# Optimization experiments

Measured on AMD Instinct MI355X. Metric: run time of the kernel, lower is better.

## Reference

```python
import jax, jax.numpy as jnp
import numpy as np

ANNEALING_SCALE = 0.1
BS, NV, S, D, V = 2, 16, 1024, 768, 50257

def setup_inputs() -> dict:
    key = jax.random.key(0)
    k1, k2, k3, k4, k5 = jax.random.split(key, 5)
    return {
        "input_ids": jax.random.randint(k1, (BS, S), 0, V),
        "content": jax.random.normal(k2, (BS, NV, S, D), dtype=jnp.float32),
        "contextualization": jax.random.normal(k3, (BS, NV, S, S), dtype=jnp.float32) * 0.05,
        "lm_head_weight": jax.random.normal(k4, (V, D), dtype=jnp.float32) * 0.02,
        "content_weights": jax.random.uniform(k5, (V, NV), dtype=jnp.float32),
    }

def reference(input_ids, content, contextualization, lm_head_weight, content_weights):
    bs, nv, s, d = content.shape
    # --- mask_annealing ---
    # Original computes relu(content @ W.T) over full vocab then gathers at input_ids.
    # Equivalent: gather rows of W first, then contract (same math since relu is
    # elementwise and only gathered columns are summed).
    Wg = lm_head_weight[input_ids]                              # (bs, s, d)
    sims = jnp.einsum('bkid,bjd->bkij', content, Wg)            # (bs, 16, s, s)
    sims = jnp.sum(jax.nn.relu(sims), axis=3)                   # (bs, 16, s)
    scores = jax.nn.sigmoid(-ANNEALING_SCALE * sims + 6.0)
    # upweight_nearby modifier
    scores = scores * (1.0 + jnp.arange(s, dtype=content.dtype) / 100.0)[None, None, :]
    scores = jnp.transpose(scores, (0, 2, 1))                   # (bs, s, 16)
    # --- create_content_soft_mask ---
    cw = content_weights[input_ids]                             # (bs, s, 16)
    weights = cw * scores + (1.0 - scores)                      # (bs, s, 16)
    # --- weighted sense combination ---
    content_m = content * jnp.transpose(weights, (0, 2, 1))[..., None]  # (bs,16,s,d)
    hidden = jnp.einsum('bkij,bkjd->bid', contextualization, content_m) # (bs, s, d)
    logits = hidden @ lm_head_weight.T                          # (bs, s, vocab)
    return logits
```

## Files before the change

### kernel.cpp

```cpp
#include <hip/hip_runtime.h>
#include <cstdint>
#include <cstddef>

#define BSZ 2
#define NV 16
#define SEQ 1024
#define DIM 768
#define VOC 50257
#define VOCP 50304

typedef unsigned int u32;
typedef unsigned short u16;
typedef _Float16 half8 __attribute__((ext_vector_type(8)));
typedef float f32x4 __attribute__((ext_vector_type(4)));

__device__ __forceinline__ u16 f2h(float f) {
  return __builtin_bit_cast(unsigned short, (_Float16)f);
}
__device__ __forceinline__ u32 pk2h(float a, float b) {
  return (u32)f2h(a) | ((u32)f2h(b) << 16);
}

__device__ __forceinline__ void gload16(const u16* g, u16* l) {
  __builtin_amdgcn_global_load_lds(
      (const __attribute__((address_space(1))) void*)g,
      (__attribute__((address_space(3))) void*)l, 16, 0, 0);
}

__global__ void k_prep_content(const float* __restrict__ content,
                               u16* __restrict__ cbf, u16* __restrict__ cT) {
  __shared__ u16 tile[64][70];
  const int bk = blockIdx.z;
  const int d0 = blockIdx.x * 64, j0 = blockIdx.y * 64;
  const float* src = content + (size_t)bk * SEQ * DIM;
  u16* dst = cbf + (size_t)bk * SEQ * DIM;
  u16* dstT = cT + (size_t)bk * DIM * SEQ;
  const int c4 = (threadIdx.x & 15) * 4;
  const int r0 = threadIdx.x >> 4;
#pragma unroll
  for (int it = 0; it < 4; ++it) {
    const int r = it * 16 + r0;
    const float4 f = *(const float4*)(src + (size_t)(j0 + r) * DIM + d0 + c4);
    const u32 lo = pk2h(f.x, f.y), hi = pk2h(f.z, f.w);
    *(uint2*)(dst + (size_t)(j0 + r) * DIM + d0 + c4) = make_uint2(lo, hi);
    *(u32*)&tile[r][c4] = lo;
    *(u32*)&tile[r][c4 + 2] = hi;
  }
  __syncthreads();
#pragma unroll
  for (int it = 0; it < 4; ++it) {
    const int dd = it * 16 + r0;
    const int j4 = c4;
    const u32 lo = (u32)tile[j4][dd] | ((u32)tile[j4 + 1][dd] << 16);
    const u32 hi = (u32)tile[j4 + 2][dd] | ((u32)tile[j4 + 3][dd] << 16);
    *(uint2*)(dstT + (size_t)(d0 + dd) * SEQ + j0 + j4) = make_uint2(lo, hi);
  }
}

__global__ void k_prep_w(const float* __restrict__ W, u16* __restrict__ Wb) {
  const int v = blockIdx.x;
  const int c = threadIdx.x * 4;
  u32 lo, hi;
  if (v < VOC) {
    const float4 f = *(const float4*)(W + (size_t)v * DIM + c);
    lo = pk2h(f.x, f.y); hi = pk2h(f.z, f.w);
  } else {
    lo = 0u; hi = 0u;
  }
  *(uint2*)(Wb + (size_t)v * DIM + c) = make_uint2(lo, hi);
}

__global__ void k_gather(const int* __restrict__ ids, const u16* __restrict__ Wb,
                         u16* __restrict__ Wg) {
  const int b = blockIdx.y, j = blockIdx.x;
  const int row = ids[b * SEQ + j];
  const int c = threadIdx.x * 4;
  *(uint2*)(Wg + ((size_t)b * SEQ + j) * DIM + c) =
      *(const uint2*)(Wb + (size_t)row * DIM + c);
}

__global__ void k_zero(float* __restrict__ p, int n) {
  const int i = blockIdx.x * 256 + threadIdx.x;
  if (i < n) p[i] = 0.f;
}

template <int LDA, int LDB>
__device__ __forceinline__ void gemm_ring1(const u16* __restrict__ A,
                                           const u16* __restrict__ B,
                                           u16* As, u16* Bs,
                                           f32x4 (&acc)[4][4], int t) {
  const int lane = t & 63, w = t >> 6, wr = w >> 1, wc = w & 1;
  const int rl = lane & 15;
  const int gsw = (((lane >> 4) ^ ((rl >> 1) & 3)) * 8);
  const int srow = 16 * w + (lane >> 2);
  const int sg = (((lane & 3) ^ ((lane >> 3) & 3)) * 8);
  const size_t gaBase = (size_t)srow * LDA + sg;
  const size_t gbBase = (size_t)srow * LDB + sg;
  const int wof = w * 512;

#define STG1_(ss, kt)                                                   \
  {                                                                     \
    const u16* ga_ = A + gaBase + (size_t)(kt) * 32;                    \
    const u16* gb_ = B + gbBase + (size_t)(kt) * 32;                    \
    gload16(ga_, As + (ss) * 4096 + wof);                               \
    gload16(ga_ + (size_t)64 * LDA, As + (ss) * 4096 + wof + 2048);     \
    gload16(gb_, Bs + (ss) * 4096 + wof);                               \
    gload16(gb_ + (size_t)64 * LDB, Bs + (ss) * 4096 + wof + 2048);     \
  }

  STG1_(0, 0);
  STG1_(1, 1);
#pragma unroll 1
  for (int kt = 0; kt < 32; ++kt) {
    if (kt < 31)
      asm volatile("s_waitcnt vmcnt(4)" ::: "memory");
    else
      asm volatile("s_waitcnt vmcnt(0)" ::: "memory");
    __builtin_amdgcn_s_barrier();
    __builtin_amdgcn_sched_barrier(0);
    const int ss = kt % 3;
    if (kt < 30) STG1_((kt + 2) % 3, kt + 2);
    half8 af[4], bf[4];
#pragma unroll
    for (int m = 0; m < 4; ++m)
      af[m] = *(const half8*)(As + ss * 4096 + (wr * 64 + m * 16 + rl) * 32 + gsw);
#pragma unroll
    for (int n = 0; n < 4; ++n)
      bf[n] = *(const half8*)(Bs + ss * 4096 + (wc * 64 + n * 16 + rl) * 32 + gsw);
    __builtin_amdgcn_s_setprio(1);
#pragma unroll
    for (int m = 0; m < 4; ++m)
#pragma unroll
      for (int n = 0; n < 4; ++n)
        acc[m][n] = __builtin_amdgcn_mfma_f32_16x16x32_f16(af[m], bf[n], acc[m][n], 0, 0, 0);
    __builtin_amdgcn_s_setprio(0);
  }
#undef STG1_
}

template <int LDA, int LDB>
__device__ __forceinline__ void gemm_ring2(const u16* __restrict__ A0,
                                           const u16* __restrict__ A1,
                                           const u16* __restrict__ B, int ksteps,
                                           u16* As0, u16* As1, u16* Bs,
                                           f32x4 (&acc0)[4][4],
                                           f32x4 (&acc1)[4][4], int t) {
  const int lane = t & 63, w = t >> 6, wr = w >> 1, wc = w & 1;
  const int rl = lane & 15;
  const int gsw = (((lane >> 4) ^ ((rl >> 1) & 3)) * 8);
  const int srow = 16 * w + (lane >> 2);
  const int sg = (((lane & 3) ^ ((lane >> 3) & 3)) * 8);
  const size_t gaBase = (size_t)srow * LDA + sg;
  const size_t gbBase = (size_t)srow * LDB + sg;
  const int wof = w * 512;

#define STG3_(ss, kt)                                                   \
  {                                                                     \
    const u16* ga0_ = A0 + gaBase + (size_t)(kt) * 32;                  \
    const u16* ga1_ = A1 + gaBase + (size_t)(kt) * 32;                  \
    const u16* gb_ = B + gbBase + (size_t)(kt) * 32;                    \
    gload16(ga0_, As0 + (ss) * 4096 + wof);                             \
    gload16(ga0_ + (size_t)64 * LDA, As0 + (ss) * 4096 + wof + 2048);   \
    gload16(ga1_, As1 + (ss) * 4096 + wof);                            \
    gload16(ga1_ + (size_t)64 * LDA, As1 + (ss) * 4096 + wof + 2048);   \
    gload16(gb_, Bs + (ss) * 4096 + wof);                              \
    gload16(gb_ + (size_t)64 * LDB, Bs + (ss) * 4096 + wof + 2048);     \
  }

#define FRAGS3_(ss)                                                     \
  half8 af0[4], af1[4], bf[4];                                          \
  _Pragma("unroll") for (int n = 0; n < 4; ++n)                         \
      bf[n] = *(const half8*)(Bs + (ss) * 4096 +                        \
                              (wc * 64 + n * 16 + rl) * 32 + gsw);      \
  _Pragma("unroll") for (int m = 0; m < 4; ++m)                         \
      af0[m] = *(const half8*)(As0 + (ss) * 4096 +                      \
                               (wr * 64 + m * 16 + rl) * 32 + gsw);     \
  _Pragma("unroll") for (int m = 0; m < 4; ++m)                         \
      af1[m] = *(const half8*)(As1 + (ss) * 4096 +                      \
                               (wr * 64 + m * 16 + rl) * 32 + gsw);

#define MFMA32_                                                         \
  __builtin_amdgcn_s_setprio(1);                                        \
  _Pragma("unroll") for (int m = 0; m < 4; ++m)                         \
      _Pragma("unroll") for (int n = 0; n < 4; ++n)                     \
          acc0[m][n] = __builtin_amdgcn_mfma_f32_16x16x32_f16(          \
              af0[m], bf[n], acc0[m][n], 0, 0, 0);                      \
  _Pragma("unroll") for (int m = 0; m < 4; ++m)                         \
      _Pragma("unroll") for (int n = 0; n < 4; ++n)                     \
          acc1[m][n] = __builtin_amdgcn_mfma_f32_16x16x32_f16(          \
              af1[m], bf[n], acc1[m][n], 0, 0, 0);                      \
  __builtin_amdgcn_s_setprio(0);

#define STEPF_(ss, kt)                                                  \
  asm volatile("s_waitcnt vmcnt(6)" ::: "memory");                      \
  __builtin_amdgcn_s_barrier();                                         \
  __builtin_amdgcn_sched_barrier(0);                                    \
  STG3_(((ss) + 2) % 3, (kt) + 2);                                      \
  { FRAGS3_(ss) MFMA32_ }

#define STEPL6_(ss)                                                     \
  asm volatile("s_waitcnt vmcnt(6)" ::: "memory");                      \
  __builtin_amdgcn_s_barrier();                                         \
  __builtin_amdgcn_sched_barrier(0);                                    \
  { FRAGS3_(ss) MFMA32_ }

#define STEPL0_(ss)                                                     \
  asm volatile("s_waitcnt vmcnt(0)" ::: "memory");                      \
  __builtin_amdgcn_s_barrier();                                         \
  __builtin_amdgcn_sched_barrier(0);                                    \
  { FRAGS3_(ss) MFMA32_ }

  STG3_(0, 0);
  STG3_(1, 1);
  const int nTrip = ksteps / 3;
  for (int u = 0; u < nTrip - 1; ++u) {
    const int kt = 3 * u;
    STEPF_(0, kt);
    STEPF_(1, kt + 1);
    STEPF_(2, kt + 2);
  }
  STEPF_(0, ksteps - 3);
  STEPL6_(1);
  STEPL0_(2);
#undef STG3_
#undef FRAGS3_
#undef MFMA32_
#undef STEPF_
#undef STEPL6_
#undef STEPL0_
}

__global__ __launch_bounds__(256, 2) void k_sims(const u16* __restrict__ cbf,
                                                 const u16* __restrict__ Wg,
                                                 float* __restrict__ sims) {
  __shared__ __align__(16) u16 As0[3 * 4096];
  __shared__ __align__(16) u16 As1[3 * 4096];
  __shared__ __align__(16) u16 Bs[3 * 4096];
  const int bk = blockIdx.z, b = bk >> 4;
  const int t = threadIdx.x;
  const int i0 = blockIdx.y * 256;
  const u16* A0 = cbf + (size_t)bk * SEQ * DIM + (size_t)i0 * DIM;
  const u16* A1 = A0 + (size_t)128 * DIM;
  const u16* B = Wg + (size_t)b * SEQ * DIM + (size_t)(blockIdx.x * 128) * DIM;
  f32x4 acc0[4][4] = {}, acc1[4][4] = {};
  gemm_ring2<DIM, DIM>(A0, A1, B, DIM / 32, As0, As1, Bs, acc0, acc1, t);
  const int lane = t & 63, w = t >> 6, wr = w >> 1;
  const int rg = lane >> 4, cl = lane & 15;
#pragma unroll
  for (int m = 0; m < 4; ++m) {
#pragma unroll
    for (int r = 0; r < 4; ++r) {
      float s0 = 0.f, s1 = 0.f;
#pragma unroll
      for (int n = 0; n < 4; ++n) {
        s0 += fmaxf(acc0[m][n][r], 0.f);
        s1 += fmaxf(acc1[m][n][r], 0.f);
      }
      s0 += __shfl_xor(s0, 1); s1 += __shfl_xor(s1, 1);
      s0 += __shfl_xor(s0, 2); s1 += __shfl_xor(s1, 2);
      s0 += __shfl_xor(s0, 4); s1 += __shfl_xor(s1, 4);
      s0 += __shfl_xor(s0, 8); s1 += __shfl_xor(s1, 8);
      if (cl == 0) {
        const int i = i0 + wr * 64 + m * 16 + rg * 4 + r;
        atomicAdd(&sims[(size_t)bk * SEQ + i], s0);
        atomicAdd(&sims[(size_t)bk * SEQ + i + 128], s1);
      }
    }
  }
}

__global__ void k_weights(const float* __restrict__ sims, const int* __restrict__ ids,
                          const float* __restrict__ cw, float* __restrict__ wtsT) {
  const int j = blockIdx.x * 256 + threadIdx.x;
  const int bk = blockIdx.y;
  const int b = bk >> 4, k = bk & 15;
  const float sm = sims[(size_t)bk * SEQ + j];
  float score = 1.f / (1.f + __expf(0.1f * sm - 6.f));
  score *= 1.f + (float)j * 0.01f;
  const int id = ids[b * SEQ + j];
  const float c = cw[(size_t)id * NV + k];
  wtsT[(size_t)bk * SEQ + j] = c * score + (1.f - score);
}

__global__ void k_ctx(const float* __restrict__ ctx, const float* __restrict__ wtsT,
                      u16* __restrict__ ctxw) {
  const size_t i = ((size_t)blockIdx.x * 256 + threadIdx.x) * 4;
  const float4 c = *(const float4*)(ctx + i);
  const size_t bk = i >> 20;
  const int j = (int)(i & (SEQ - 1));
  const float4 wv = *(const float4*)(wtsT + bk * SEQ + j);
  *(uint2*)(ctxw + i) =
      make_uint2(pk2h(c.x * wv.x, c.y * wv.y), pk2h(c.z * wv.z, c.w * wv.w));
}

__global__ __launch_bounds__(256, 2) void k_hidden(const u16* __restrict__ ctxw,
                                                   const u16* __restrict__ cT,
                                                   float* __restrict__ part) {
  __shared__ __align__(16) u16 As[3 * 4096];
  __shared__ __align__(16) u16 Bs[3 * 4096];
  const int z = blockIdx.z;
  const int b = z >> 2, g = z & 3;
  const int i0 = blockIdx.y * 128, d0 = blockIdx.x * 128;
  const int t = threadIdx.x;
  f32x4 acc[4][4] = {};
  for (int kk = 0; kk < 4; ++kk) {
    const int sense = g * 4 + kk;
    const u16* A = ctxw + ((size_t)(b * NV + sense) * SEQ + i0) * SEQ;
    const u16* B = cT + ((size_t)(b * NV + sense) * DIM + d0) * SEQ;
    gemm_ring1<SEQ, SEQ>(A, B, As, Bs, acc, t);
    __syncthreads();
  }
  const int lane = t & 63, w = t >> 6, wr = w >> 1, wc = w & 1;
  const int rg = lane >> 4, cl = lane & 15;
  float* P = part + ((size_t)(g * BSZ + b) * SEQ + i0) * DIM + d0;
#pragma unroll
  for (int m = 0; m < 4; ++m)
#pragma unroll
    for (int n = 0; n < 4; ++n)
#pragma unroll
      for (int r = 0; r < 4; ++r)
        P[(size_t)(wr * 64 + m * 16 + rg * 4 + r) * DIM + wc * 64 + n * 16 + cl] =
            acc[m][n][r];
}

__global__ void k_reduce(const float* __restrict__ part, u16* __restrict__ hid) {
  const size_t i = ((size_t)blockIdx.x * 256 + threadIdx.x) * 4;
  const size_t NHID = (size_t)BSZ * SEQ * DIM;
  float4 s = {0.f, 0.f, 0.f, 0.f};
#pragma unroll
  for (int g = 0; g < 4; ++g) {
    const float4 p = *(const float4*)(part + (size_t)g * NHID + i);
    s.x += p.x; s.y += p.y; s.z += p.z; s.w += p.w;
  }
  *(uint2*)(hid + i) = make_uint2(pk2h(s.x, s.y), pk2h(s.z, s.w));
}

__global__ __launch_bounds__(512, 2) void k_logits(const u16* __restrict__ hid,
                                                   const u16* __restrict__ Wb,
                                                   float* __restrict__ out) {
  __shared__ __align__(16) u16 lds[8 * 8192];
  const int bid = blockIdx.x;
  const int swz = (bid & 7) * 197 + (bid >> 3);
  const int it = swz & 7, vt = swz >> 3;
  const int i0 = it * 256;
  const int v0 = (vt == 196) ? (VOCP - 256) : vt * 256;
  const int t = threadIdx.x;
  const int lane = t & 63, w = t >> 6;
  const int wm = w >> 2, wn = w & 3;
  const int rl = lane & 15, kg = lane >> 4;
  const int gsw = (kg ^ ((rl >> 1) & 3)) * 8;
  const int srow = t >> 2;
  const int sgr = ((t & 3) ^ ((srow >> 1) & 3)) * 8;
  const u16* Abase = hid + (size_t)i0 * DIM;
  const u16* Bbase = Wb + (size_t)v0 * DIM;
  u16* ldst = lds + w * 512 + lane * 8;

#define STG(slot, base, koff)                                         \
  {                                                                   \
    const u16* s_ = (base) + (size_t)srow * DIM + (koff) + sgr;       \
    gload16(s_, ldst + (slot) * 8192);                                \
    gload16(s_ + (size_t)128 * DIM, ldst + (slot) * 8192 + 4096);     \
  }

#define SCHED0 __builtin_amdgcn_sched_barrier(0)
#define VM8 asm volatile("s_waitcnt vmcnt(8)" ::: "memory")
#define VM4 asm volatile("s_waitcnt vmcnt(4)" ::: "memory")
#define VM0 asm volatile("s_waitcnt vmcnt(0)" ::: "memory")
#define VMX
#define LGKM0 asm volatile("s_waitcnt lgkmcnt(0)" ::: "memory"); SCHED0

#define RD_BF(sB)                                                     \
  _Pragma("unroll") for (int n = 0; n < 4; ++n)                       \
      bf[n] = *(const half8*)(lds + (sB) * 8192 +                     \
                              (wn * 64 + n * 16 + rl) * 32 + gsw);
#define RD_AF(sA, mo)                                                 \
  _Pragma("unroll") for (int m = 0; m < 4; ++m)                       \
      af[m] = *(const half8*)(lds + (sA) * 8192 +                     \
                              (wm * 128 + ((mo) + m) * 16 + rl) * 32 + gsw);
#define MF16(mo)                                                      \
  __builtin_amdgcn_s_setprio(1);                                      \
  _Pragma("unroll") for (int m = 0; m < 4; ++m)                       \
      _Pragma("unroll") for (int n = 0; n < 4; ++n)                   \
          acc[(mo) + m][n] = __builtin_amdgcn_mfma_f32_16x16x32_f16(  \
              af[m], bf[n], acc[(mo) + m][n], 0, 0, 0);               \
  __builtin_amdgcn_s_setprio(0);

#define SLICE(sA, sB, stA, stB, koff, VMW)                            \
  {                                                                   \
    half8 af[4], bf[4];                                               \
    RD_BF(sB); RD_AF(sA, 0);                                          \
    STG(stA, Abase, koff);                                            \
    SCHED0; __builtin_amdgcn_s_barrier();                             \
    LGKM0; MF16(0);                                                   \
    SCHED0; __builtin_amdgcn_s_barrier();                             \
    RD_AF(sA, 4);                                                     \
    STG(stB, Bbase, koff);                                            \
    SCHED0; __builtin_amdgcn_s_barrier();                             \
    LGKM0; MF16(4);                                                   \
    VMW;                                                              \
    SCHED0; __builtin_amdgcn_s_barrier();                             \
  }

#define SLICE_NS(sA, sB, VMW)                                         \
  {                                                                   \
    half8 af[4], bf[4];                                               \
    RD_BF(sB); RD_AF(sA, 0);                                          \
    SCHED0; __builtin_amdgcn_s_barrier();                             \
    LGKM0; MF16(0);                                                   \
    SCHED0; __builtin_amdgcn_s_barrier();                             \
    RD_AF(sA, 4);                                                     \
    SCHED0; __builtin_amdgcn_s_barrier();                             \
    LGKM0; MF16(4);                                                   \
    VMW;                                                              \
    SCHED0; __builtin_amdgcn_s_barrier();                             \
  }

  f32x4 acc[8][4] = {};
  STG(0, Abase, 0);
  STG(1, Bbase, 0);
  STG(2, Abase, 32);
  STG(3, Bbase, 32);
  STG(4, Abase, 64);
  STG(5, Bbase, 64);
  VM8;
  __builtin_amdgcn_s_barrier();
  SCHED0;

#pragma unroll 1
  for (int g = 0; g < 5; ++g) {
    const int kb = g * 128;
    SLICE(0, 1, 6, 7, kb + 96, VM8);
    SLICE(2, 3, 0, 1, kb + 128, VM8);
    SLICE(4, 5, 2, 3, kb + 160, VM8);
    SLICE(6, 7, 4, 5, kb + 192, VM8);
  }
  SLICE(0, 1, 6, 7, 736, VM8);
  SLICE_NS(2, 3, VM4);
  SLICE_NS(4, 5, VM0);
  SLICE_NS(6, 7, VMX);
#undef STG
#undef SLICE
#undef SLICE_NS
#undef RD_BF
#undef RD_AF
#undef MF16
#undef LGKM0
#undef VM8
#undef VM4
#undef VM0
#undef VMX
#undef SCHED0

#pragma unroll
  for (int m = 0; m < 8; ++m)
#pragma unroll
    for (int n = 0; n < 4; ++n) {
      const int vv = v0 + wn * 64 + n * 16 + rl;
      if (vv < VOC) {
        const int ib = i0 + wm * 128 + m * 16 + kg * 4;
#pragma unroll
        for (int r = 0; r < 4; ++r)
          out[(size_t)(ib + r) * VOC + vv] = acc[m][n][r];
      }
    }
}

extern "C" void kernel_launch(void* const* d_in, const int* in_sizes, int n_in,
                              void* d_out, int out_size, void* d_ws, size_t ws_size,
                              hipStream_t stream) {
  const int* ids = (const int*)d_in[0];
  const float* content = (const float*)d_in[1];
  const float* ctx = (const float*)d_in[2];
  const float* W = (const float*)d_in[3];
  const float* cw = (const float*)d_in[4];
  float* out = (float*)d_out;
  char* ws = (char*)d_ws;

  u16* cbf  = (u16*)(ws);
  u16* cT   = (u16*)(ws + 50331648);
  u16* Wb   = (u16*)(ws + 100663296);
  u16* Wg   = (u16*)(ws + 177930240);
  u16* ctxw = (u16*)(ws + 181075968);
  float* sims = (float*)(ws + 248184832);
  float* wtsT = (float*)(ws + 248315904);
  float* part = (float*)cbf;
  u16* hid = Wg;

  k_prep_content<<<dim3(DIM / 64, SEQ / 64, BSZ * NV), 256, 0, stream>>>(
      content, cbf, cT);
  k_prep_w<<<VOCP, 192, 0, stream>>>(W, Wb);
  k_gather<<<dim3(SEQ, BSZ), 192, 0, stream>>>(ids, Wb, Wg);
  k_zero<<<128, 256, 0, stream>>>(sims, BSZ * NV * SEQ);
  k_sims<<<dim3(8, 4, BSZ * NV), 256, 0, stream>>>(cbf, Wg, sims);
  k_weights<<<dim3(4, BSZ * NV), 256, 0, stream>>>(sims, ids, cw, wtsT);
  k_ctx<<<32768, 256, 0, stream>>>(ctx, wtsT, ctxw);
  k_hidden<<<dim3(6, 8, 8), 256, 0, stream>>>(ctxw, cT, part);
  k_reduce<<<1536, 256, 0, stream>>>(part, hid);
  k_logits<<<8 * 197, 512, 0, stream>>>(hid, Wb, out);
}
```

Before: 580.6 us.

## Split hidden GEMM over more sense groups and retile logits GEMM to 256x128

The hidden-state GEMM now splits the 16 senses into 8 groups of 2 instead of 4 groups of 4. This doubles the grid and the number of partial buffers the reduce kernel sums, and raises the launch-bounds occupancy hint. The logits GEMM drops from 512-thread 256x256 tiles with an 8-slot split A/B LDS ring to 256-thread 256x128 tiles. Those tiles use a 3-stage combined A+B ring with one barrier per k-step. The aim is better CU balance and fewer barriers, at the cost of more partial-sum traffic and less B reuse per block.

```diff
diff --git a/kernel.cpp b/kernel.cpp
--- a/kernel.cpp
+++ b/kernel.cpp
@@ -293,18 +293,18 @@
       make_uint2(pk2h(c.x * wv.x, c.y * wv.y), pk2h(c.z * wv.z, c.w * wv.w));
 }
 
-__global__ __launch_bounds__(256, 2) void k_hidden(const u16* __restrict__ ctxw,
+__global__ __launch_bounds__(256, 3) void k_hidden(const u16* __restrict__ ctxw,
                                                    const u16* __restrict__ cT,
                                                    float* __restrict__ part) {
   __shared__ __align__(16) u16 As[3 * 4096];
   __shared__ __align__(16) u16 Bs[3 * 4096];
   const int z = blockIdx.z;
-  const int b = z >> 2, g = z & 3;
+  const int b = z >> 3, g = z & 7;
   const int i0 = blockIdx.y * 128, d0 = blockIdx.x * 128;
   const int t = threadIdx.x;
   f32x4 acc[4][4] = {};
-  for (int kk = 0; kk < 4; ++kk) {
-    const int sense = g * 4 + kk;
+  for (int kk = 0; kk < 2; ++kk) {
+    const int sense = g * 2 + kk;
     const u16* A = ctxw + ((size_t)(b * NV + sense) * SEQ + i0) * SEQ;
     const u16* B = cT + ((size_t)(b * NV + sense) * DIM + d0) * SEQ;
     gemm_ring1<SEQ, SEQ>(A, B, As, Bs, acc, t);
@@ -328,128 +328,93 @@
   const size_t NHID = (size_t)BSZ * SEQ * DIM;
   float4 s = {0.f, 0.f, 0.f, 0.f};
 #pragma unroll
-  for (int g = 0; g < 4; ++g) {
+  for (int g = 0; g < 8; ++g) {
     const float4 p = *(const float4*)(part + (size_t)g * NHID + i);
     s.x += p.x; s.y += p.y; s.z += p.z; s.w += p.w;
   }
   *(uint2*)(hid + i) = make_uint2(pk2h(s.x, s.y), pk2h(s.z, s.w));
 }
 
-__global__ __launch_bounds__(512, 2) void k_logits(const u16* __restrict__ hid,
+__global__ __launch_bounds__(256, 2) void k_logits(const u16* __restrict__ hid,
                                                    const u16* __restrict__ Wb,
                                                    float* __restrict__ out) {
-  __shared__ __align__(16) u16 lds[8 * 8192];
+  __shared__ __align__(16) u16 lds[3 * 12288];
   const int bid = blockIdx.x;
-  const int swz = (bid & 7) * 197 + (bid >> 3);
+  const int swz = (bid & 7) * 393 + (bid >> 3);
   const int it = swz & 7, vt = swz >> 3;
-  const int i0 = it * 256;
-  const int v0 = (vt == 196) ? (VOCP - 256) : vt * 256;
+  const int i0 = it * 256, v0 = vt * 128;
   const int t = threadIdx.x;
   const int lane = t & 63, w = t >> 6;
-  const int wm = w >> 2, wn = w & 3;
+  const int wm = w >> 1, wn = w & 1;
   const int rl = lane & 15, kg = lane >> 4;
   const int gsw = (kg ^ ((rl >> 1) & 3)) * 8;
   const int srow = t >> 2;
   const int sgr = ((t & 3) ^ ((srow >> 1) & 3)) * 8;
-  const u16* Abase = hid + (size_t)i0 * DIM;
-  const u16* Bbase = Wb + (size_t)v0 * DIM;
-  u16* ldst = lds + w * 512 + lane * 8;
-
-#define STG(slot, base, koff)                                         \
+  const u16* Abase = hid + ((size_t)i0 + srow) * DIM + sgr;
+  const u16* Bbase = Wb + ((size_t)v0 + srow) * DIM + sgr;
+  u16* dls = lds + t * 8;
+
+#define STG(ss, koff)                                                 \
   {                                                                   \
-    const u16* s_ = (base) + (size_t)srow * DIM + (koff) + sgr;       \
-    gload16(s_, ldst + (slot) * 8192);                                \
-    gload16(s_ + (size_t)128 * DIM, ldst + (slot) * 8192 + 4096);     \
-  }
-
-#define SCHED0 __builtin_amdgcn_sched_barrier(0)
-#define VM8 asm volatile("s_waitcnt vmcnt(8)" ::: "memory")
-#define VM4 asm volatile("s_waitcnt vmcnt(4)" ::: "memory")
-#define VM0 asm volatile("s_waitcnt vmcnt(0)" ::: "memory")
-#define VMX
-#define LGKM0 asm volatile("s_waitcnt lgkmcnt(0)" ::: "memory"); SCHED0
-
-#define RD_BF(sB)                                                     \
-  _Pragma("unroll") for (int n = 0; n < 4; ++n)                       \
-      bf[n] = *(const half8*)(lds + (sB) * 8192 +                     \
-                              (wn * 64 + n * 16 + rl) * 32 + gsw);
-#define RD_AF(sA, mo)                                                 \
-  _Pragma("unroll") for (int m = 0; m < 4; ++m)                       \
-      af[m] = *(const half8*)(lds + (sA) * 8192 +                     \
-                              (wm * 128 + ((mo) + m) * 16 + rl) * 32 + gsw);
-#define MF16(mo)                                                      \
-  __builtin_amdgcn_s_setprio(1);                                      \
-  _Pragma("unroll") for (int m = 0; m < 4; ++m)                       \
-      _Pragma("unroll") for (int n = 0; n < 4; ++n)                   \
-          acc[(mo) + m][n] = __builtin_amdgcn_mfma_f32_16x16x32_f16(  \
-              af[m], bf[n], acc[(mo) + m][n], 0, 0, 0);               \
-  __builtin_amdgcn_s_setprio(0);
-
-#define SLICE(sA, sB, stA, stB, koff, VMW)                            \
+    const u16* a_ = Abase + (koff);                                   \
+    u16* d_ = dls + (ss) * 12288;                                     \
+    gload16(a_, d_);                                                  \
+    gload16(a_ + (size_t)64 * DIM, d_ + 2048);                        \
+    gload16(a_ + (size_t)128 * DIM, d_ + 4096);                       \
+    gload16(a_ + (size_t)192 * DIM, d_ + 6144);                       \
+    const u16* b_ = Bbase + (koff);                                   \
+    gload16(b_, d_ + 8192);                                           \
+    gload16(b_ + (size_t)64 * DIM, d_ + 10240);                       \
+  }
+
+#define CMP(ss)                                                       \
   {                                                                   \
-    half8 af[4], bf[4];                                               \
-    RD_BF(sB); RD_AF(sA, 0);                                          \
-    STG(stA, Abase, koff);                                            \
-    SCHED0; __builtin_amdgcn_s_barrier();                             \
-    LGKM0; MF16(0);                                                   \
-    SCHED0; __builtin_amdgcn_s_barrier();                             \
-    RD_AF(sA, 4);                                                     \
-    STG(stB, Bbase, koff);                                            \
-    SCHED0; __builtin_amdgcn_s_barrier();                             \
-    LGKM0; MF16(4);                                                   \
-    VMW;                                                              \
-    SCHED0; __builtin_amdgcn_s_barrier();                             \
-  }
-
-#define SLICE_NS(sA, sB, VMW)                                         \
-  {                                                                   \
-    half8 af[4], bf[4];                                               \
-    RD_BF(sB); RD_AF(sA, 0);                                          \
-    SCHED0; __builtin_amdgcn_s_barrier();                             \
-    LGKM0; MF16(0);                                                   \
-    SCHED0; __builtin_amdgcn_s_barrier();                             \
-    RD_AF(sA, 4);                                                     \
-    SCHED0; __builtin_amdgcn_s_barrier();                             \
-    LGKM0; MF16(4);                                                   \
-    VMW;                                                              \
-    SCHED0; __builtin_amdgcn_s_barrier();                             \
-  }
+    half8 af[8], bf[4];                                               \
+    _Pragma("unroll") for (int n = 0; n < 4; ++n)                     \
+        bf[n] = *(const half8*)(lds + (ss) * 12288 + 8192 +           \
+                                (wn * 64 + n * 16 + rl) * 32 + gsw);  \
+    _Pragma("unroll") for (int m = 0; m < 8; ++m)                     \
+        af[m] = *(const half8*)(lds + (ss) * 12288 +                  \
+                                (wm * 128 + m * 16 + rl) * 32 + gsw); \
+    __builtin_amdgcn_s_setprio(1);                                    \
+    _Pragma("unroll") for (int m = 0; m < 8; ++m)                     \
+        _Pragma("unroll") for (int n = 0; n < 4; ++n)                 \
+            acc[m][n] = __builtin_amdgcn_mfma_f32_16x16x32_f16(       \
+                af[m], bf[n], acc[m][n], 0, 0, 0);                    \
+    __builtin_amdgcn_s_setprio(0);                                    \
+  }
+
+#define BARS                                                          \
+  __builtin_amdgcn_s_barrier();                                       \
+  __builtin_amdgcn_sched_barrier(0);
+
+#define STEPF(ss, st, koff)                                           \
+  asm volatile("s_waitcnt vmcnt(6)" ::: "memory");                    \
+  BARS;                                                               \
+  STG(st, koff);                                                      \
+  CMP(ss)
 
   f32x4 acc[8][4] = {};
-  STG(0, Abase, 0);
-  STG(1, Bbase, 0);
-  STG(2, Abase, 32);
-  STG(3, Bbase, 32);
-  STG(4, Abase, 64);
-  STG(5, Bbase, 64);
-  VM8;
-  __builtin_amdgcn_s_barrier();
-  SCHED0;
-
+  STG(0, 0);
+  STG(1, 32);
 #pragma unroll 1
-  for (int g = 0; g < 5; ++g) {
-    const int kb = g * 128;
-    SLICE(0, 1, 6, 7, kb + 96, VM8);
-    SLICE(2, 3, 0, 1, kb + 128, VM8);
-    SLICE(4, 5, 2, 3, kb + 160, VM8);
-    SLICE(6, 7, 4, 5, kb + 192, VM8);
-  }
-  SLICE(0, 1, 6, 7, 736, VM8);
-  SLICE_NS(2, 3, VM4);
-  SLICE_NS(4, 5, VM0);
-  SLICE_NS(6, 7, VMX);
+  for (int u = 0; u < 7; ++u) {
+    const int kb = u * 96;
+    STEPF(0, 2, kb + 64);
+    STEPF(1, 0, kb + 96);
+    STEPF(2, 1, kb + 128);
+  }
+  STEPF(0, 2, 736);
+  asm volatile("s_waitcnt vmcnt(6)" ::: "memory");
+  BARS;
+  CMP(1);
+  asm volatile("s_waitcnt vmcnt(0)" ::: "memory");
+  BARS;
+  CMP(2);
 #undef STG
-#undef SLICE
-#undef SLICE_NS
-#undef RD_BF
-#undef RD_AF
-#undef MF16
-#undef LGKM0
-#undef VM8
-#undef VM4
-#undef VM0
-#undef VMX
-#undef SCHED0
+#undef CMP
+#undef BARS
+#undef STEPF
 
 #pragma unroll
   for (int m = 0; m < 8; ++m)
@@ -494,7 +459,7 @@
   k_sims<<<dim3(8, 4, BSZ * NV), 256, 0, stream>>>(cbf, Wg, sims);
   k_weights<<<dim3(4, BSZ * NV), 256, 0, stream>>>(sims, ids, cw, wtsT);
   k_ctx<<<32768, 256, 0, stream>>>(ctx, wtsT, ctxw);
-  k_hidden<<<dim3(6, 8, 8), 256, 0, stream>>>(ctxw, cT, part);
+  k_hidden<<<dim3(6, 8, 16), 256, 0, stream>>>(ctxw, cT, part);
   k_reduce<<<1536, 256, 0, stream>>>(part, hid);
-  k_logits<<<8 * 197, 512, 0, stream>>>(hid, Wb, out);
-}
+  k_logits<<<8 * 393, 256, 0, stream>>>(hid, Wb, out);
+}
```

After: 564.1 us. 1.03x faster.
